# Kernel tuning notes

Measured on AMD Instinct MI355X. Metric: run time of the kernel, lower is better.

## Reference

```python
import jax, jax.numpy as jnp
import numpy as np
from jax import lax

D = 4            # shift radius
NSHIFT = 2 * D + 1  # 9 shifts per axis -> 81 total


def setup_inputs() -> dict:
    key = jax.random.key(0)
    k1, k2, k3, k4, k5, k6 = jax.random.split(key, 6)
    B, C, H, W = 4, 256, 64, 128
    R = 16  # reduction ratio
    feat1 = jax.random.normal(k1, (B, C, H, W), dtype=jnp.float32)
    feat2 = jax.random.normal(k2, (B, C, H, W), dtype=jnp.float32)
    # ca_conv1: Conv2d(C, C//R, 1) -> weight [C//R, C], bias [C//R]
    w1 = jax.random.normal(k3, (C // R, C), dtype=jnp.float32) * (1.0 / np.sqrt(C))
    b1 = jax.random.normal(k4, (C // R,), dtype=jnp.float32) * 0.01
    # ca_conv2: Conv2d(C//R, C, 1) -> weight [C, C//R], bias [C]
    w2 = jax.random.normal(k5, (C, C // R), dtype=jnp.float32) * (1.0 / np.sqrt(C // R))
    b2 = jax.random.normal(k6, (C,), dtype=jnp.float32) * 0.01
    return {"feat1": feat1, "feat2": feat2, "w1": w1, "b1": b1, "w2": w2, "b2": b2}


def reference(feat1, feat2, w1, b1, w2, b2):
    B, C, H, W = feat1.shape
    # zero-pad feat2 spatially by D on each side (matches F.pad constant 0)
    feat2p = jnp.pad(feat2, ((0, 0), (0, 0), (D, D), (D, D)))

    def one_shift(carry, idx):
        i = idx // NSHIFT
        j = idx % NSHIFT
        f2 = lax.dynamic_slice(feat2p, (0, 0, i, j), (B, C, H, W))
        sim = feat1 * f2                              # [B,C,H,W]
        pooled = jnp.mean(sim, axis=(2, 3))           # global avg pool -> [B,C]
        a = pooled @ w1.T + b1                        # [B,C//R] (1x1 conv == matmul)
        a = a @ w2.T + b2                             # [B,C]
        a = jax.nn.sigmoid(a)
        out = jnp.mean(a[:, :, None, None] * sim, axis=1)  # channel mean -> [B,H,W]
        return carry, out

    _, cv = lax.scan(one_shift, None, jnp.arange(NSHIFT * NSHIFT))  # [81,B,H,W]
    return jnp.transpose(cv, (1, 0, 2, 3))  # [B,81,H,W]
```

## Files before the change

### kernel.cpp

```cpp
#include <hip/hip_runtime.h>
#include <math.h>


#define HH 64
#define WW 128
#define CC 256
#define BB 4

__global__ __launch_bounds__(576, 6) void corr_pool_kernel(
    const float* __restrict__ f1, const float* __restrict__ f2,
    float* __restrict__ pooled) {
  const int t  = threadIdx.x;
  const int bc = blockIdx.x;
  const float* f1p = f1 + (size_t)bc * (HH * WW);
  const float* f2p = f2 + (size_t)bc * (HH * WW);

  __shared__ float4 f2s4[72 * 35];
  float* red = (float*)f2s4;

  const float4 z4 = make_float4(0.f, 0.f, 0.f, 0.f);
  for (int u = t; u < 72 * 35; u += 576) {
    const int rl = u / 35, k = u - rl * 35;
    const int gr = rl - 4;
    float4 v = z4;
    if ((unsigned)gr < 64u && k >= 1 && k <= 32)
      v = *(const float4*)(f2p + (gr << 7) + ((k - 1) << 2));
    f2s4[u] = v;
  }
  __syncthreads();

  const int h  = t / 9;
  const int di = t - h * 9;
  const float4* f2row = &f2s4[(h + di) * 35];
  const float* f1row  = f1p + (h << 7);

  float s9[9];
#pragma unroll
  for (int j = 0; j < 9; ++j) s9[j] = 0.f;

#pragma unroll 2
  for (int seg = 0; seg < 8; ++seg) {
    const int w0 = seg << 4;
    alignas(16) float f1r[16];
#pragma unroll
    for (int m = 0; m < 4; ++m)
      *(float4*)&f1r[4 * m] = *(const float4*)(f1row + w0 + (m << 2));

    alignas(16) float f2w[24];
#pragma unroll
    for (int m = 0; m < 6; ++m) *(float4*)&f2w[4 * m] = f2row[(seg << 2) + m];

#pragma unroll
    for (int k = 0; k < 16; ++k) {
      const float a = f1r[k];
#pragma unroll
      for (int j = 0; j < 9; ++j) s9[j] += a * f2w[k + j];
    }
  }

  __syncthreads();
#pragma unroll
  for (int j = 0; j < 9; ++j) red[h * 81 + di * 9 + j] = s9[j];
  __syncthreads();

  if (t < 81) {
    float acc = 0.f;
#pragma unroll 8
    for (int hh = 0; hh < 64; ++hh) acc += red[hh * 81 + t];
    const int b = bc >> 8, c = bc & 255;
    pooled[(size_t)(b * 81 + t) * 256 + c] = acc;
  }
}

__global__ __launch_bounds__(256) void mlp_kernel(
    const float* __restrict__ pooled, const float* __restrict__ w1,
    const float* __restrict__ b1, const float* __restrict__ w2,
    const float* __restrict__ b2, float* __restrict__ At) {
  const int bs = blockIdx.x;
  const int t  = threadIdx.x;
  const int b  = bs / 81;
  const int s  = bs - b * 81;
  __shared__ float p[256];
  __shared__ float hid[16];

  p[t] = pooled[(size_t)bs * 256 + t] * (1.0f / 8192.0f);
  __syncthreads();

  const int g = t >> 4, ln = t & 15;
  float acc = 0.f;
#pragma unroll
  for (int m = 0; m < 16; ++m) {
    const int c = (m << 4) + ln;
    acc += w1[(g << 8) + c] * p[c];
  }
  acc += __shfl_xor(acc, 1);
  acc += __shfl_xor(acc, 2);
  acc += __shfl_xor(acc, 4);
  acc += __shfl_xor(acc, 8);
  if (ln == 0) hid[g] = acc + b1[g];
  __syncthreads();

  float acc2 = b2[t];
#pragma unroll
  for (int k = 0; k < 16; ++k) acc2 += w2[(t << 4) + k] * hid[k];
  const float sv = 1.0f / (1.0f + __expf(-acc2));
  At[((size_t)(b * 256 + t)) * 81 + s] = sv;
}

__global__ __launch_bounds__(64, 4) void out_kernel(
    const float* __restrict__ f1, const float* __restrict__ f2,
    const float* __restrict__ At, float* __restrict__ out,
    float* __restrict__ part) {
  const int bid  = blockIdx.x;
  const int x    = bid & 7;
  const int q    = bid >> 3;
  const int i    = q % 9;
  const int tq   = q / 9;
  const int tile = tq * 8 + x;
  const int half = tile & 1;
  const int rt   = (tile >> 1) & 31;
  const int b    = tile >> 6;
  const int h0   = rt << 1;

  const int t    = threadIdx.x;
  const int r    = t >> 5;
  const int cidx = t & 31;
  const int w0   = cidx << 2;
  const int h    = h0 + r;
  const int hr   = h + i - 4;
  const bool rowok = ((unsigned)hr < 64u);

  float acc[9][4];
#pragma unroll
  for (int j = 0; j < 9; ++j)
#pragma unroll
    for (int k = 0; k < 4; ++k) acc[j][k] = 0.f;

  if (rowok) {
    const int c0 = half << 7;
    const float* p1 = f1 + (size_t)b * (CC * 8192) + (size_t)c0 * 8192 +
                      (h << 7) + w0;
    const float* p2 = f2 + (size_t)b * (CC * 8192) + (size_t)c0 * 8192 +
                      (hr << 7);
    const float* Ab = At + (size_t)b * (CC * 81) + (size_t)c0 * 81 + i * 9;

    const bool vA  = (cidx > 0);
    const bool vC  = (cidx < 31);
    const int ofsA = vA ? (w0 - 4) : 0;
    const int ofsC = vC ? (w0 + 4) : 120;

    float4 nx = *(const float4*)(p1);
    float4 nA = *(const float4*)(p2 + ofsA);
    float4 nB = *(const float4*)(p2 + w0);
    float4 nC = *(const float4*)(p2 + ofsC);

    for (int c = 0; c < 128; ++c) {
      const float4 xv = nx, fA = nA, fB = nB, fC = nC;
      const int adv = (c < 127) ? 8192 : 0;
      p1 += adv;
      p2 += adv;
      nx = *(const float4*)(p1);
      nA = *(const float4*)(p2 + ofsA);
      nB = *(const float4*)(p2 + w0);
      nC = *(const float4*)(p2 + ofsC);

      alignas(16) float f2r[12];
      f2r[0] = vA ? fA.x : 0.f;
      f2r[1] = vA ? fA.y : 0.f;
      f2r[2] = vA ? fA.z : 0.f;
      f2r[3] = vA ? fA.w : 0.f;
      f2r[4] = fB.x; f2r[5] = fB.y; f2r[6] = fB.z; f2r[7] = fB.w;
      f2r[8]  = vC ? fC.x : 0.f;
      f2r[9]  = vC ? fC.y : 0.f;
      f2r[10] = vC ? fC.z : 0.f;
      f2r[11] = vC ? fC.w : 0.f;

      alignas(16) const float xx[4] = {xv.x, xv.y, xv.z, xv.w};

      const float* avp = Ab + (size_t)c * 81;
#pragma unroll
      for (int j = 0; j < 9; ++j) {
        const float wj = avp[j];
#pragma unroll
        for (int k = 0; k < 4; ++k) acc[j][k] += wj * (xx[k] * f2r[k + j]);
      }
    }
  }

  float* dst = half ? part : out;
  const float inv = 1.0f / 256.0f;
#pragma unroll
  for (int j = 0; j < 9; ++j) {
    float4 o;
    o.x = acc[j][0] * inv;
    o.y = acc[j][1] * inv;
    o.z = acc[j][2] * inv;
    o.w = acc[j][3] * inv;
    *(float4*)(dst + (((size_t)(b * 81 + i * 9 + j) * 64 + h) << 7) + w0) = o;
  }
}

__global__ __launch_bounds__(256) void combine_kernel(
    float* __restrict__ out, const float* __restrict__ part) {
  const size_t idx = (size_t)blockIdx.x * 256 + threadIdx.x;
  float4* o4       = (float4*)out;
  const float4* p4 = (const float4*)part;
  const float4 a = o4[idx], p = p4[idx];
  float4 rv;
  rv.x = a.x + p.x; rv.y = a.y + p.y; rv.z = a.z + p.z; rv.w = a.w + p.w;
  o4[idx] = rv;
}

extern "C" void kernel_launch(void* const* d_in, const int* in_sizes, int n_in,
                              void* d_out, int out_size, void* d_ws, size_t ws_size,
                              hipStream_t stream) {
  const float* feat1 = (const float*)d_in[0];
  const float* feat2 = (const float*)d_in[1];
  const float* w1    = (const float*)d_in[2];
  const float* b1    = (const float*)d_in[3];
  const float* w2    = (const float*)d_in[4];
  const float* b2    = (const float*)d_in[5];
  float* out = (float*)d_out;

  float* pooled = (float*)d_ws;
  float* At     = pooled + 82944;
  float* cpart  = At + 82944;

  corr_pool_kernel<<<1024, 576, 0, stream>>>(feat1, feat2, pooled);
  mlp_kernel<<<4 * 81, 256, 0, stream>>>(pooled, w1, b1, w2, b2, At);
  out_kernel<<<2304, 64, 0, stream>>>(feat1, feat2, At, out, cpart);
  combine_kernel<<<2592, 256, 0, stream>>>(out, cpart);
}
```

Baseline: 195.9 us.

## Split channel reduction across waves in-block and drop combine kernel

The output kernel now uses 256-thread blocks in which four wavefronts each handle 64 channels and reduce their partial sums through shared memory. This replaces the two-half split that wrote a partial buffer and needed a separate combine kernel. The change removes the extra global write and read of the full output-sized partial and one kernel launch. The pooling kernel also gets a two-level shared-memory reduction over rows, and its launch bound drops the occupancy hint. Costs are fewer blocks (1152), an extra barrier and LDS traffic in the output kernel, and possible register-pressure changes.

```diff
diff --git a/kernel.cpp b/kernel.cpp
--- a/kernel.cpp
+++ b/kernel.cpp
@@ -7,7 +7,7 @@
 #define CC 256
 #define BB 4
 
-__global__ __launch_bounds__(576, 6) void corr_pool_kernel(
+__global__ __launch_bounds__(576) void corr_pool_kernel(
     const float* __restrict__ f1, const float* __restrict__ f2,
     float* __restrict__ pooled) {
   const int t  = threadIdx.x;
@@ -16,7 +16,6 @@
   const float* f2p = f2 + (size_t)bc * (HH * WW);
 
   __shared__ float4 f2s4[72 * 35];
-  float* red = (float*)f2s4;
 
   const float4 z4 = make_float4(0.f, 0.f, 0.f, 0.f);
   for (int u = t; u < 72 * 35; u += 576) {
@@ -59,14 +58,26 @@
   }
 
   __syncthreads();
+  float* red  = (float*)f2s4;
+  float* red2 = red + 64 * 81;
 #pragma unroll
   for (int j = 0; j < 9; ++j) red[h * 81 + di * 9 + j] = s9[j];
+  __syncthreads();
+
+  if (t < 567) {
+    const int col = t % 81, g = t / 81;
+    const int r0 = g * 9, r1 = (g == 6) ? 64 : r0 + 9;
+    float acc = 0.f;
+#pragma unroll 3
+    for (int rr = r0; rr < r1; ++rr) acc += red[rr * 81 + col];
+    red2[g * 81 + col] = acc;
+  }
   __syncthreads();
 
   if (t < 81) {
     float acc = 0.f;
-#pragma unroll 8
-    for (int hh = 0; hh < 64; ++hh) acc += red[hh * 81 + t];
+#pragma unroll
+    for (int g = 0; g < 7; ++g) acc += red2[g * 81 + t];
     const int b = bc >> 8, c = bc & 255;
     pooled[(size_t)(b * 81 + t) * 256 + c] = acc;
   }
@@ -107,29 +118,31 @@
   At[((size_t)(b * 256 + t)) * 81 + s] = sv;
 }
 
-__global__ __launch_bounds__(64, 4) void out_kernel(
+__global__ __launch_bounds__(256, 5) void out_kernel(
     const float* __restrict__ f1, const float* __restrict__ f2,
-    const float* __restrict__ At, float* __restrict__ out,
-    float* __restrict__ part) {
+    const float* __restrict__ At, float* __restrict__ out) {
   const int bid  = blockIdx.x;
   const int x    = bid & 7;
   const int q    = bid >> 3;
   const int i    = q % 9;
   const int tq   = q / 9;
   const int tile = tq * 8 + x;
-  const int half = tile & 1;
-  const int rt   = (tile >> 1) & 31;
-  const int b    = tile >> 6;
+  const int b    = tile >> 5;
+  const int rt   = tile & 31;
   const int h0   = rt << 1;
 
   const int t    = threadIdx.x;
-  const int r    = t >> 5;
-  const int cidx = t & 31;
+  const int wv   = t >> 6;
+  const int l    = t & 63;
+  const int r    = l >> 5;
+  const int cidx = l & 31;
   const int w0   = cidx << 2;
   const int h    = h0 + r;
   const int hr   = h + i - 4;
   const bool rowok = ((unsigned)hr < 64u);
 
+  __shared__ float redbuf[3][64][36];
+
   float acc[9][4];
 #pragma unroll
   for (int j = 0; j < 9; ++j)
@@ -137,7 +150,7 @@
     for (int k = 0; k < 4; ++k) acc[j][k] = 0.f;
 
   if (rowok) {
-    const int c0 = half << 7;
+    const int c0 = wv << 6;
     const float* p1 = f1 + (size_t)b * (CC * 8192) + (size_t)c0 * 8192 +
                       (h << 7) + w0;
     const float* p2 = f2 + (size_t)b * (CC * 8192) + (size_t)c0 * 8192 +
@@ -154,9 +167,9 @@
     float4 nB = *(const float4*)(p2 + w0);
     float4 nC = *(const float4*)(p2 + ofsC);
 
-    for (int c = 0; c < 128; ++c) {
+    for (int c = 0; c < 64; ++c) {
       const float4 xv = nx, fA = nA, fB = nB, fC = nC;
-      const int adv = (c < 127) ? 8192 : 0;
+      const int adv = (c < 63) ? 8192 : 0;
       p1 += adv;
       p2 += adv;
       nx = *(const float4*)(p1);
@@ -187,28 +200,33 @@
     }
   }
 
-  float* dst = half ? part : out;
-  const float inv = 1.0f / 256.0f;
-#pragma unroll
-  for (int j = 0; j < 9; ++j) {
-    float4 o;
-    o.x = acc[j][0] * inv;
-    o.y = acc[j][1] * inv;
-    o.z = acc[j][2] * inv;
-    o.w = acc[j][3] * inv;
-    *(float4*)(dst + (((size_t)(b * 81 + i * 9 + j) * 64 + h) << 7) + w0) = o;
-  }
-}
-
-__global__ __launch_bounds__(256) void combine_kernel(
-    float* __restrict__ out, const float* __restrict__ part) {
-  const size_t idx = (size_t)blockIdx.x * 256 + threadIdx.x;
-  float4* o4       = (float4*)out;
-  const float4* p4 = (const float4*)part;
-  const float4 a = o4[idx], p = p4[idx];
-  float4 rv;
-  rv.x = a.x + p.x; rv.y = a.y + p.y; rv.z = a.z + p.z; rv.w = a.w + p.w;
-  o4[idx] = rv;
+  if (wv > 0) {
+#pragma unroll
+    for (int j = 0; j < 9; ++j)
+#pragma unroll
+      for (int k = 0; k < 4; ++k) redbuf[wv - 1][l][j * 4 + k] = acc[j][k];
+  }
+  __syncthreads();
+
+  if (wv == 0) {
+#pragma unroll
+    for (int qq = 0; qq < 3; ++qq)
+#pragma unroll
+      for (int j = 0; j < 9; ++j)
+#pragma unroll
+        for (int k = 0; k < 4; ++k) acc[j][k] += redbuf[qq][l][j * 4 + k];
+
+    const float inv = 1.0f / 256.0f;
+#pragma unroll
+    for (int j = 0; j < 9; ++j) {
+      float4 o;
+      o.x = acc[j][0] * inv;
+      o.y = acc[j][1] * inv;
+      o.z = acc[j][2] * inv;
+      o.w = acc[j][3] * inv;
+      *(float4*)(out + (((size_t)(b * 81 + i * 9 + j) * 64 + h) << 7) + w0) = o;
+    }
+  }
 }
 
 extern "C" void kernel_launch(void* const* d_in, const int* in_sizes, int n_in,
@@ -224,10 +242,8 @@
 
   float* pooled = (float*)d_ws;
   float* At     = pooled + 82944;
-  float* cpart  = At + 82944;
 
   corr_pool_kernel<<<1024, 576, 0, stream>>>(feat1, feat2, pooled);
   mlp_kernel<<<4 * 81, 256, 0, stream>>>(pooled, w1, b1, w2, b2, At);
-  out_kernel<<<2304, 64, 0, stream>>>(feat1, feat2, At, out, cpart);
-  combine_kernel<<<2592, 256, 0, stream>>>(out, cpart);
-}
+  out_kernel<<<1152, 256, 0, stream>>>(feat1, feat2, At, out);
+}
```

New measurement: 335.7 us. +71.4%, slower.

## Deepen software prefetch in correlation kernels and parallelize pooled reduction

Applied to the files above, without the earlier changes.

Both main kernels now prefetch further ahead. corr_pool double-buffers its f1/f2 register segments, and out_kernel keeps two channels of global loads in flight and prefetches the attention weights into registers. The final 64-row reduction in corr_pool is split across 567 threads in two stages instead of 81 serial threads. The launch-bounds occupancy hint on corr_pool is dropped. The deeper pipelines raise register pressure, which may lower occupancy or cause spills.

```diff
diff --git a/kernel.cpp b/kernel.cpp
--- a/kernel.cpp
+++ b/kernel.cpp
@@ -7,7 +7,7 @@
 #define CC 256
 #define BB 4
 
-__global__ __launch_bounds__(576, 6) void corr_pool_kernel(
+__global__ __launch_bounds__(576) void corr_pool_kernel(
     const float* __restrict__ f1, const float* __restrict__ f2,
     float* __restrict__ pooled) {
   const int t  = threadIdx.x;
@@ -16,7 +16,6 @@
   const float* f2p = f2 + (size_t)bc * (HH * WW);
 
   __shared__ float4 f2s4[72 * 35];
-  float* red = (float*)f2s4;
 
   const float4 z4 = make_float4(0.f, 0.f, 0.f, 0.f);
   for (int u = t; u < 72 * 35; u += 576) {
@@ -38,35 +37,56 @@
 #pragma unroll
   for (int j = 0; j < 9; ++j) s9[j] = 0.f;
 
-#pragma unroll 2
+  alignas(16) float f1c[16], f2wc[24];
+#pragma unroll
+  for (int m = 0; m < 4; ++m)
+    *(float4*)&f1c[4 * m] = *(const float4*)(f1row + (m << 2));
+#pragma unroll
+  for (int m = 0; m < 6; ++m) *(float4*)&f2wc[4 * m] = f2row[m];
+
   for (int seg = 0; seg < 8; ++seg) {
-    const int w0 = seg << 4;
-    alignas(16) float f1r[16];
+    const int nxt = (seg < 7) ? seg + 1 : 7;
+    alignas(16) float f1n[16], f2wn[24];
 #pragma unroll
     for (int m = 0; m < 4; ++m)
-      *(float4*)&f1r[4 * m] = *(const float4*)(f1row + w0 + (m << 2));
-
-    alignas(16) float f2w[24];
-#pragma unroll
-    for (int m = 0; m < 6; ++m) *(float4*)&f2w[4 * m] = f2row[(seg << 2) + m];
+      *(float4*)&f1n[4 * m] =
+          *(const float4*)(f1row + (nxt << 4) + (m << 2));
+#pragma unroll
+    for (int m = 0; m < 6; ++m) *(float4*)&f2wn[4 * m] = f2row[(nxt << 2) + m];
 
 #pragma unroll
     for (int k = 0; k < 16; ++k) {
-      const float a = f1r[k];
-#pragma unroll
-      for (int j = 0; j < 9; ++j) s9[j] += a * f2w[k + j];
+      const float a = f1c[k];
+#pragma unroll
+      for (int j = 0; j < 9; ++j) s9[j] += a * f2wc[k + j];
     }
-  }
-
-  __syncthreads();
+#pragma unroll
+    for (int m = 0; m < 16; ++m) f1c[m] = f1n[m];
+#pragma unroll
+    for (int m = 0; m < 24; ++m) f2wc[m] = f2wn[m];
+  }
+
+  __syncthreads();
+  float* red  = (float*)f2s4;
+  float* red2 = red + 64 * 81;
 #pragma unroll
   for (int j = 0; j < 9; ++j) red[h * 81 + di * 9 + j] = s9[j];
+  __syncthreads();
+
+  if (t < 567) {
+    const int col = t % 81, g = t / 81;
+    const int r0 = g * 9, r1 = (g == 6) ? 64 : r0 + 9;
+    float acc = 0.f;
+#pragma unroll 3
+    for (int rr = r0; rr < r1; ++rr) acc += red[rr * 81 + col];
+    red2[g * 81 + col] = acc;
+  }
   __syncthreads();
 
   if (t < 81) {
     float acc = 0.f;
-#pragma unroll 8
-    for (int hh = 0; hh < 64; ++hh) acc += red[hh * 81 + t];
+#pragma unroll
+    for (int g = 0; g < 7; ++g) acc += red2[g * 81 + t];
     const int b = bc >> 8, c = bc & 255;
     pooled[(size_t)(b * 81 + t) * 256 + c] = acc;
   }
@@ -149,41 +169,58 @@
     const int ofsA = vA ? (w0 - 4) : 0;
     const int ofsC = vC ? (w0 + 4) : 120;
 
-    float4 nx = *(const float4*)(p1);
-    float4 nA = *(const float4*)(p2 + ofsA);
-    float4 nB = *(const float4*)(p2 + w0);
-    float4 nC = *(const float4*)(p2 + ofsC);
+    float4 s0x = *(const float4*)(p1);
+    float4 s0A = *(const float4*)(p2 + ofsA);
+    float4 s0B = *(const float4*)(p2 + w0);
+    float4 s0C = *(const float4*)(p2 + ofsC);
+    p1 += 8192; p2 += 8192;
+    float4 s1x = *(const float4*)(p1);
+    float4 s1A = *(const float4*)(p2 + ofsA);
+    float4 s1B = *(const float4*)(p2 + w0);
+    float4 s1C = *(const float4*)(p2 + ofsC);
+
+    float av[9];
+#pragma unroll
+    for (int j = 0; j < 9; ++j) av[j] = Ab[j];
+    const float* qa = Ab + 81;
 
     for (int c = 0; c < 128; ++c) {
-      const float4 xv = nx, fA = nA, fB = nB, fC = nC;
-      const int adv = (c < 127) ? 8192 : 0;
-      p1 += adv;
-      p2 += adv;
-      nx = *(const float4*)(p1);
-      nA = *(const float4*)(p2 + ofsA);
-      nB = *(const float4*)(p2 + w0);
-      nC = *(const float4*)(p2 + ofsC);
+      const int adv = (c < 126) ? 8192 : 0;
+      p1 += adv; p2 += adv;
+      const float4 nx = *(const float4*)(p1);
+      const float4 nA = *(const float4*)(p2 + ofsA);
+      const float4 nB = *(const float4*)(p2 + w0);
+      const float4 nC = *(const float4*)(p2 + ofsC);
+
+      float avn[9];
+#pragma unroll
+      for (int j = 0; j < 9; ++j) avn[j] = qa[j];
 
       alignas(16) float f2r[12];
-      f2r[0] = vA ? fA.x : 0.f;
-      f2r[1] = vA ? fA.y : 0.f;
-      f2r[2] = vA ? fA.z : 0.f;
-      f2r[3] = vA ? fA.w : 0.f;
-      f2r[4] = fB.x; f2r[5] = fB.y; f2r[6] = fB.z; f2r[7] = fB.w;
-      f2r[8]  = vC ? fC.x : 0.f;
-      f2r[9]  = vC ? fC.y : 0.f;
-      f2r[10] = vC ? fC.z : 0.f;
-      f2r[11] = vC ? fC.w : 0.f;
-
-      alignas(16) const float xx[4] = {xv.x, xv.y, xv.z, xv.w};
-
-      const float* avp = Ab + (size_t)c * 81;
+      f2r[0] = vA ? s0A.x : 0.f;
+      f2r[1] = vA ? s0A.y : 0.f;
+      f2r[2] = vA ? s0A.z : 0.f;
+      f2r[3] = vA ? s0A.w : 0.f;
+      f2r[4] = s0B.x; f2r[5] = s0B.y; f2r[6] = s0B.z; f2r[7] = s0B.w;
+      f2r[8]  = vC ? s0C.x : 0.f;
+      f2r[9]  = vC ? s0C.y : 0.f;
+      f2r[10] = vC ? s0C.z : 0.f;
+      f2r[11] = vC ? s0C.w : 0.f;
+
+      alignas(16) const float xx[4] = {s0x.x, s0x.y, s0x.z, s0x.w};
+
 #pragma unroll
       for (int j = 0; j < 9; ++j) {
-        const float wj = avp[j];
+        const float wj = av[j];
 #pragma unroll
         for (int k = 0; k < 4; ++k) acc[j][k] += wj * (xx[k] * f2r[k + j]);
       }
+
+      s0x = s1x; s0A = s1A; s0B = s1B; s0C = s1C;
+      s1x = nx;  s1A = nA;  s1B = nB;  s1C = nC;
+#pragma unroll
+      for (int j = 0; j < 9; ++j) av[j] = avn[j];
+      qa += (c < 126) ? 81 : 0;
     }
   }
 
```

Result: no change. 197.8 us (+0.9%).
